# Kernel tuning notes

Measured on AMD Instinct MI355X. Metric: run time of the kernel, lower is better.

The kernel has to match this reference:

```python
import jax, jax.numpy as jnp
import numpy as np

EPS = 1e-8
INV_SQRT = 1.0 / np.sqrt(1.0 + EPS)  # 1/sqrt(|k|+eps), |k|=1 for both hyp and sph


def layernorm(x, w, b, eps=1e-5):
    m = jnp.mean(x, axis=-1, keepdims=True)
    v = jnp.mean((x - m) ** 2, axis=-1, keepdims=True)
    return (x - m) * jax.lax.rsqrt(v + eps) * w + b


def setup_inputs() -> dict:
    key = jax.random.key(0)
    B, S, D, H = 4, 1024, 512, 8
    d = D // H
    FF = 2048
    ks = jax.random.split(key, 12)
    s_attn = 1.0 / np.sqrt(d)
    s_d = 1.0 / np.sqrt(D)
    s_ff = 1.0 / np.sqrt(FF)
    return {
        "x": jax.random.normal(ks[0], (B, S, D), jnp.float32),
        "Wq": jax.random.normal(ks[1], (H, d, d), jnp.float32) * s_attn,
        "Wk": jax.random.normal(ks[2], (H, d, d), jnp.float32) * s_attn,
        "Wv": jax.random.normal(ks[3], (H, d, d), jnp.float32) * s_attn,
        "gw": jnp.ones((H, 3), jnp.float32) / 3.0,
        "temp": jnp.ones((H,), jnp.float32),
        "Wo": jax.random.normal(ks[4], (D, D), jnp.float32) * s_d,
        "bo": jnp.zeros((D,), jnp.float32),
        "ln1_w": jnp.ones((D,), jnp.float32),
        "ln1_b": jnp.zeros((D,), jnp.float32),
        "ln2_w": jnp.ones((D,), jnp.float32),
        "ln2_b": jnp.zeros((D,), jnp.float32),
        "W1": jax.random.normal(ks[5], (FF, D), jnp.float32) * s_d,
        "b1": jnp.zeros((FF,), jnp.float32),
        "W2": jax.random.normal(ks[6], (D, FF), jnp.float32) * s_ff,
        "b2": jnp.zeros((D,), jnp.float32),
    }


def reference(x, Wq, Wk, Wv, gw, temp, Wo, bo, ln1_w, ln1_b, ln2_w, ln2_b, W1, b1, W2, b2):
    B, S, D = x.shape
    H = Wq.shape[0]
    d = D // H

    h = layernorm(x, ln1_w, ln1_b)
    xh = h.reshape(B, S, H, d).transpose(0, 2, 1, 3)  # [B,H,S,d]
    # nn.Linear: y = x @ W^T
    q = jnp.einsum("bhsd,hed->bhse", xh, Wq)
    k = jnp.einsum("bhsd,hed->bhse", xh, Wk)
    v = jnp.einsum("bhsd,hed->bhse", xh, Wv)

    qsq = jnp.sum(q * q, axis=-1)  # [B,H,S] == ||q||^2
    ksq = jnp.sum(k * k, axis=-1)
    qk = jnp.einsum("bhsd,bhtd->bhst", q, k)
    # ||q-k||^2 via expansion (same math as sum(diff^2), avoids [B,H,S,S,d])
    dsq = jnp.maximum(qsq[..., :, None] + ksq[..., None, :] - 2.0 * qk, 0.0)
    euc = jnp.sqrt(dsq + EPS)

    denom = (1.0 - qsq)[..., :, None] * (1.0 - ksq)[..., None, :] + EPS
    cosh_arg = jnp.clip(1.0 + 2.0 * dsq / denom, 1.0, 1e6)
    hyp = jnp.arccosh(cosh_arg) * INV_SQRT

    qn = jnp.sqrt(qsq)
    kn = jnp.sqrt(ksq)
    cos_angle = qk / ((qn + EPS)[..., :, None] * (kn + EPS)[..., None, :])
    cos_angle = jnp.clip(cos_angle, -1.0 + EPS, 1.0 - EPS)
    sph = jnp.arccos(cos_angle) * INV_SQRT

    w = jax.nn.softmax(gw, axis=-1)  # [H,3] per-head geometry mixing
    comb = (
        w[:, 0, None, None] * hyp
        + w[:, 1, None, None] * euc
        + w[:, 2, None, None] * sph
    )
    sim = -comb * temp[None, :, None, None]
    attn = jax.nn.softmax(sim, axis=-1)
    out = jnp.einsum("bhst,bhtd->bhsd", attn, v)
    out = out.transpose(0, 2, 1, 3).reshape(B, S, D)
    attn_out = out @ Wo.T + bo

    x = x + attn_out  # dropout=0 (eval)
    h2 = layernorm(x, ln2_w, ln2_b)
    ff = jax.nn.gelu(h2 @ W1.T + b1, approximate=False) @ W2.T + b2
    return x + ff, w
```

## Files before the change

kernel.cpp:

```cpp
#include <hip/hip_runtime.h>
#include <hip/hip_bf16.h>
#include <math.h>

typedef __attribute__((ext_vector_type(4))) float f32x4;
typedef __attribute__((ext_vector_type(8))) short bf16x8;
typedef unsigned short u16;
typedef unsigned int u32;

typedef f32x4  __attribute__((may_alias)) f32x4a;
typedef bf16x8 __attribute__((may_alias)) bf16x8a;
typedef uint2  __attribute__((may_alias)) uint2a;

__device__ __forceinline__ u16 bfbits(float f) {
  union { __hip_bfloat16 h; u16 u; } cv;
  cv.h = __float2bfloat16(f);
  return cv.u;
}
__device__ __forceinline__ float rcp_r(float x)  { return __builtin_amdgcn_rcpf(x); }
__device__ __forceinline__ float sqrt_r(float x) { return __builtin_amdgcn_sqrtf(x); }
__device__ __forceinline__ float log2_r(float x) { return __builtin_amdgcn_logf(x); }
__device__ __forceinline__ float exp2_r(float x) { return __builtin_amdgcn_exp2f(x); }
__device__ __forceinline__ float rsq_r(float x)  { return __builtin_amdgcn_rsqf(x); }
__device__ __forceinline__ u32 cvt_pk_bf16(float lo, float hi) {
  u32 r;
  asm("v_cvt_pk_bf16_f32 %0, %1, %2" : "=v"(r) : "v"(lo), "v"(hi));
  return r;
}
typedef const __attribute__((address_space(1))) unsigned int* gas_t;
typedef __attribute__((address_space(3))) unsigned int* las_t;
__device__ __forceinline__ void gload_lds16(const u16* g, u16* l) {
  __builtin_amdgcn_global_load_lds((gas_t)g, (las_t)l, 16, 0, 0);
}

__global__ __launch_bounds__(256) void convert_weights(
    const float* __restrict__ wq, const float* __restrict__ wk, const float* __restrict__ wv,
    const float* __restrict__ wo, const float* __restrict__ w1, const float* __restrict__ w2,
    u16* __restrict__ owq, u16* __restrict__ owk, u16* __restrict__ owv,
    u16* __restrict__ owo, u16* __restrict__ ow1, u16* __restrict__ ow2) {
  int i = blockIdx.x * 256 + threadIdx.x;
  const float* src; u16* dst; int base;
  if (i < 8192)        { src = wq; dst = owq; base = 0; }
  else if (i < 16384)  { src = wk; dst = owk; base = 8192; }
  else if (i < 24576)  { src = wv; dst = owv; base = 16384; }
  else if (i < 90112)  { src = wo; dst = owo; base = 24576; }
  else if (i < 352256) { src = w1; dst = ow1; base = 90112; }
  else                 { src = w2; dst = ow2; base = 352256; }
  int li = i - base;
  float4 v = reinterpret_cast<const float4*>(src)[li];
  ushort4 o;
  o.x = bfbits(v.x); o.y = bfbits(v.y); o.z = bfbits(v.z); o.w = bfbits(v.w);
  reinterpret_cast<ushort4*>(dst)[li] = o;
}

__global__ __launch_bounds__(128) void ln_kernel(const float* __restrict__ x,
    const float* __restrict__ w, const float* __restrict__ b, u16* __restrict__ out) {
  int row = blockIdx.x, tid = threadIdx.x;
  float4 v = reinterpret_cast<const float4*>(x + row * 512)[tid];
  float s  = v.x + v.y + v.z + v.w;
  float s2 = v.x*v.x + v.y*v.y + v.z*v.z + v.w*v.w;
  #pragma unroll
  for (int o = 32; o > 0; o >>= 1) { s += __shfl_down(s, o); s2 += __shfl_down(s2, o); }
  __shared__ float sm[4];
  if ((tid & 63) == 0) { sm[(tid >> 6)*2] = s; sm[(tid >> 6)*2 + 1] = s2; }
  __syncthreads();
  float ts = sm[0] + sm[2], ts2 = sm[1] + sm[3];
  float mean = ts * (1.f/512.f);
  float var  = ts2 * (1.f/512.f) - mean*mean;
  float rstd = rsq_r(var + 1e-5f);
  float4 wv = reinterpret_cast<const float4*>(w)[tid];
  float4 bv = reinterpret_cast<const float4*>(b)[tid];
  ushort4 o;
  o.x = bfbits((v.x-mean)*rstd*wv.x + bv.x);
  o.y = bfbits((v.y-mean)*rstd*wv.y + bv.y);
  o.z = bfbits((v.z-mean)*rstd*wv.z + bv.z);
  o.w = bfbits((v.w-mean)*rstd*wv.w + bv.w);
  reinterpret_cast<ushort4*>(out + row * 512)[tid] = o;
}

__global__ __launch_bounds__(256) void qkv_kernel(const u16* __restrict__ h1,
    const u16* __restrict__ wqb, const u16* __restrict__ wkb, const u16* __restrict__ wvb,
    u16* __restrict__ q, u16* __restrict__ k, u16* __restrict__ vt,
    float* __restrict__ qsq, float* __restrict__ qom, float* __restrict__ qrs,
    float* __restrict__ ksq, float* __restrict__ kom, float* __restrict__ krs) {
  int mt = blockIdx.x, head = blockIdx.y;
  int wave = threadIdx.x >> 6, lane = threadIdx.x & 63;
  int lr = lane & 15, lg = lane >> 4;
  int m0 = mt * 64 + wave * 16;
  const u16* xr = h1 + (m0 + lr) * 512 + head * 64 + lg * 8;
  bf16x8 a0 = *reinterpret_cast<const bf16x8a*>(xr);
  bf16x8 a1 = *reinterpret_cast<const bf16x8a*>(xr + 32);
  int m_base = m0 + 4*lg;
  int bq = m_base >> 10;
  int s_base = m_base & 1023;
  int bh = (bq << 3) + head;
  #pragma unroll 1
  for (int mat = 0; mat < 3; ++mat) {
    const u16* W = (mat == 0 ? wqb : mat == 1 ? wkb : wvb) + head * 4096;
    f32x4 acc[4];
    #pragma unroll
    for (int c = 0; c < 4; c++)
      #pragma unroll
      for (int j = 0; j < 4; j++) acc[c][j] = 0.f;
    #pragma unroll
    for (int c = 0; c < 4; c++) {
      const u16* wr = W + (c*16 + lr) * 64 + lg * 8;
      bf16x8 b0 = *reinterpret_cast<const bf16x8a*>(wr);
      bf16x8 b1 = *reinterpret_cast<const bf16x8a*>(wr + 32);
      acc[c] = __builtin_amdgcn_mfma_f32_16x16x32_bf16(a0, b0, acc[c], 0, 0, 0);
      acc[c] = __builtin_amdgcn_mfma_f32_16x16x32_bf16(a1, b1, acc[c], 0, 0, 0);
    }
    if (mat == 2) {
      #pragma unroll
      for (int c = 0; c < 4; c++)
        #pragma unroll
        for (int j = 0; j < 4; j++)
          vt[(bh*64 + c*16 + lr) * 1024 + s_base + j] = bfbits(acc[c][j]);
    } else {
      u16* dst = (mat == 0 ? q : k);
      float* sq = (mat == 0 ? qsq : ksq);
      float* om = (mat == 0 ? qom : kom);
      float* rs = (mat == 0 ? qrs : krs);
      float ss[4] = {0.f, 0.f, 0.f, 0.f};
      #pragma unroll
      for (int c = 0; c < 4; c++)
        #pragma unroll
        for (int j = 0; j < 4; j++) {
          float vv = acc[c][j];
          dst[(bh*1024 + s_base + j) * 64 + c*16 + lr] = bfbits(vv);
          ss[j] += vv * vv;
        }
      #pragma unroll
      for (int j = 0; j < 4; j++) {
        #pragma unroll
        for (int o = 1; o < 16; o <<= 1) ss[j] += __shfl_xor(ss[j], o);
      }
      if (lr == 0) {
        #pragma unroll
        for (int j = 0; j < 4; j++) {
          float v = ss[j];
          int idx = bh*1024 + s_base + j;
          sq[idx] = v;
          om[idx] = rcp_r(1.f - v);
          rs[idx] = rsq_r(v);
        }
      }
    }
  }
}

__global__ __launch_bounds__(512, 4) void attn_kernel(
    const u16* __restrict__ q, const u16* __restrict__ k, const u16* __restrict__ vt,
    const float* __restrict__ qsqA, const float* __restrict__ qomA, const float* __restrict__ qrsA,
    const float* __restrict__ ksqA, const float* __restrict__ komA, const float* __restrict__ krsA,
    const float* __restrict__ gw, const float* __restrict__ temp,
    u16* __restrict__ attnb) {
  int bh = blockIdx.y;
  int b = bh >> 3, head = bh & 7;
  int tid = threadIdx.x;
  int wave = tid >> 6;
  int wq = wave & 1;
  int split = wave >> 1;
  int lane = tid & 63;
  int lr = lane & 15, lg = lane >> 4;
  int q0 = blockIdx.x * 32 + wq * 16;

  const u16* qp = q  + bh * 65536;
  const u16* kp = k  + bh * 65536;
  const u16* vp = vt + bh * 65536;

  __shared__ float ks_s[1024], kom_s[1024], rkn_s[1024];
  __shared__ __align__(16) u16 umem[5120];
  u16* pw = umem + wave * 640;

  for (int i = tid; i < 1024; i += 512) {
    ks_s[i]  = ksqA[(bh << 10) + i];
    kom_s[i] = komA[(bh << 10) + i];
    rkn_s[i] = krsA[(bh << 10) + i];
  }
  __syncthreads();

  float g0 = gw[head*3], g1 = gw[head*3+1], g2 = gw[head*3+2];
  float gm = fmaxf(g0, fmaxf(g1, g2));
  float e0 = __expf(g0-gm), e1 = __expf(g1-gm), e2 = __expf(g2-gm);
  float gi = rcp_r(e0 + e1 + e2);
  float tp = temp[head];
  const float LOG2E = 1.4426950408889634f;
  float chn = -e0*gi*tp;
  float cen = -e1*gi*tp*LOG2E;
  float csn = -e2*gi*tp*LOG2E;

  const u16* qr = qp + (q0 + lr) * 64 + lg * 8;
  bf16x8 aq0 = *reinterpret_cast<const bf16x8a*>(qr);
  bf16x8 aq1 = *reinterpret_cast<const bf16x8a*>(qr + 32);
  float qs   = qsqA[(bh << 10) + q0 + lr];
  float qom2 = 2.f * qomA[(bh << 10) + q0 + lr];
  float rqn  = qrsA[(bh << 10) + q0 + lr];

  f32x4 acc[4];
  #pragma unroll
  for (int c = 0; c < 4; c++)
    #pragma unroll
    for (int j = 0; j < 4; j++) acc[c][j] = 0.f;
  float psum0 = 0.f, psum1 = 0.f;

  for (int it = 0; it < 8; ++it) {
    int t0 = split * 256 + it * 32;
    const u16* kr = kp + (t0 + lr) * 64 + lg * 8;
    bf16x8 k00 = *reinterpret_cast<const bf16x8a*>(kr);
    bf16x8 k01 = *reinterpret_cast<const bf16x8a*>(kr + 32);
    bf16x8 k10 = *reinterpret_cast<const bf16x8a*>(kr + 1024);
    bf16x8 k11 = *reinterpret_cast<const bf16x8a*>(kr + 1024 + 32);
    f32x4 s0, s1;
    #pragma unroll
    for (int j = 0; j < 4; j++) { s0[j] = 0.f; s1[j] = 0.f; }
    s0 = __builtin_amdgcn_mfma_f32_16x16x32_bf16(k00, aq0, s0, 0, 0, 0);
    s0 = __builtin_amdgcn_mfma_f32_16x16x32_bf16(k01, aq1, s0, 0, 0, 0);
    s1 = __builtin_amdgcn_mfma_f32_16x16x32_bf16(k10, aq0, s1, 0, 0, 0);
    s1 = __builtin_amdgcn_mfma_f32_16x16x32_bf16(k11, aq1, s1, 0, 0, 0);

    f32x4 kq0 = *reinterpret_cast<const f32x4a*>(&ks_s[t0 + 4*lg]);
    f32x4 kq1 = *reinterpret_cast<const f32x4a*>(&ks_s[t0 + 16 + 4*lg]);
    f32x4 ko0 = *reinterpret_cast<const f32x4a*>(&kom_s[t0 + 4*lg]);
    f32x4 ko1 = *reinterpret_cast<const f32x4a*>(&kom_s[t0 + 16 + 4*lg]);
    f32x4 rk0 = *reinterpret_cast<const f32x4a*>(&rkn_s[t0 + 4*lg]);
    f32x4 rk1 = *reinterpret_cast<const f32x4a*>(&rkn_s[t0 + 16 + 4*lg]);

    float pv0[4], pv1[4];
    #pragma unroll
    for (int tc = 0; tc < 2; tc++) {
      f32x4 sv = tc ? s1 : s0;
      f32x4 kq = tc ? kq1 : kq0;
      f32x4 ko = tc ? ko1 : ko0;
      f32x4 rk = tc ? rk1 : rk0;
      float* pv = tc ? pv1 : pv0;
      #pragma unroll
      for (int j = 0; j < 4; j++) {
        float qk  = sv[j];
        float dsq = fmaxf(fmaf(qk, -2.f, qs + kq[j]), 0.f);
        float euc = sqrt_r(dsq);
        float u   = dsq * qom2 * ko[j];
        u = fminf(fmaxf(u, 0.f), 999999.f);
        float u2 = u + u;
        float sr = sqrt_r(fmaf(u, u, u2));
        float hyp2 = log2_r((u + 1.f) + sr);
        float ca = qk * rqn * rk[j];
        ca = fminf(fmaxf(ca, -1.f), 1.f);
        float aa = fabsf(ca);
        float pp = fmaf(aa, -0.0187293f, 0.0742610f);
        pp = fmaf(aa, pp, -0.2121144f);
        pp = fmaf(aa, pp, 1.5707288f);
        float rr = sqrt_r(1.f - aa) * pp;
        float sph = ca < 0.f ? 3.14159265358979f - rr : rr;
        float sim2 = fmaf(chn, hyp2, fmaf(cen, euc, csn * sph));
        float p = exp2_r(sim2);
        if (tc) psum1 += p; else psum0 += p;
        pv[j] = p;
      }
    }
    u32 w0 = cvt_pk_bf16(pv0[0], pv0[1]);
    u32 w1 = cvt_pk_bf16(pv0[2], pv0[3]);
    u32 w2 = cvt_pk_bf16(pv1[0], pv1[1]);
    u32 w3 = cvt_pk_bf16(pv1[2], pv1[3]);
    *reinterpret_cast<uint2a*>(pw + lr*40 + 4*lg)      = make_uint2(w0, w1);
    *reinterpret_cast<uint2a*>(pw + lr*40 + 16 + 4*lg) = make_uint2(w2, w3);
    bf16x8 pa = *reinterpret_cast<const bf16x8a*>(pw + lr*40 + lg*8);
    #pragma unroll
    for (int c = 0; c < 4; c++) {
      bf16x8 av = *reinterpret_cast<const bf16x8a*>(vp + (c*16 + lr)*1024 + t0 + lg*8);
      acc[c] = __builtin_amdgcn_mfma_f32_16x16x32_bf16(av, pa, acc[c], 0, 0, 0);
    }
  }

  float lt = psum0 + psum1;
  lt += __shfl_xor(lt, 16);
  lt += __shfl_xor(lt, 32);

  float* fa = (float*)umem;
  __syncthreads();
  #pragma unroll 1
  for (int s = 1; s <= 3; ++s) {
    int base = (wq*64 + lane)*20;
    if (split == s) {
      #pragma unroll
      for (int c = 0; c < 4; c++)
        *reinterpret_cast<f32x4a*>(fa + base + c*4) = acc[c];
      fa[base + 16] = lt;
    }
    __syncthreads();
    if (split == 0) {
      #pragma unroll
      for (int c = 0; c < 4; c++)
        acc[c] += *reinterpret_cast<const f32x4a*>(fa + base + c*4);
      lt += fa[base + 16];
    }
    __syncthreads();
  }
  if (split == 0) {
    float rl = rcp_r(lt);
    #pragma unroll
    for (int c = 0; c < 4; c++) {
      ushort4 st;
      st.x = bfbits(acc[c][0]*rl); st.y = bfbits(acc[c][1]*rl);
      st.z = bfbits(acc[c][2]*rl); st.w = bfbits(acc[c][3]*rl);
      *reinterpret_cast<ushort4*>(
          &attnb[(size_t)((b << 10) + q0 + lr) * 512 + head*64 + c*16 + 4*lg]) = st;
    }
  }
}

template<int K, int KS, int BM, int BN, int MODE>
__global__ __launch_bounds__(256, 2) void gemm_kernel(
    const u16* __restrict__ X, const u16* __restrict__ W,
    const float* __restrict__ bias, const float* __restrict__ res,
    float* __restrict__ outf, float* __restrict__ outf2, u16* __restrict__ outb) {
  constexpr int NS  = (MODE == 1) ? 2048 : 512;
  constexpr int WM  = (BM == 128 && BN == 128) ? 64 : 32;
  constexpr int WN  = (BN == 128 || BM == 128) ? 64 : 32;
  constexpr int NFR = WM / 16;
  constexpr int NFC = WN / 16;
  constexpr int NWC = BN / WN;
  constexpr int ACH = (BM * 4) / 256;
  constexpr int BCH = (BN * 4) / 256;
  __shared__ u16 As[BM * 32];
  __shared__ u16 Bs[BN * 32];
  int tid = threadIdx.x;
  int wave = tid >> 6, lane = tid & 63;
  int lr = lane & 15, lg = lane >> 4;
  int wr = (NWC == 2) ? (wave >> 1) : wave;
  int wc = (NWC == 2) ? (wave & 1) : 0;
  int m0 = blockIdx.x * BM, n0 = blockIdx.y * BN;
  const u16* Xp = X;
  const u16* Wp = W;
  if constexpr (MODE == 3) { Xp += blockIdx.z * K; Wp += blockIdx.z * K; }
  f32x4 acc[NFR][NFC];
  #pragma unroll
  for (int fr = 0; fr < NFR; fr++)
    #pragma unroll
    for (int fc = 0; fc < NFC; fc++)
      #pragma unroll
      for (int j = 0; j < 4; j++) acc[fr][fc][j] = 0.f;
  const u16* Ag[ACH]; u16* Al[ACH];
  const u16* Bg[BCH]; u16* Bl[BCH];
  #pragma unroll
  for (int i = 0; i < ACH; i++) {
    int cb = i * 256 + wave * 64;
    int c  = cb + lane;
    int row = c >> 2;
    int col = ((c & 3) ^ (row & 3)) << 3;
    Ag[i] = Xp + (size_t)(m0 + row) * KS + col;
    Al[i] = As + cb * 8;
  }
  #pragma unroll
  for (int i = 0; i < BCH; i++) {
    int cb = i * 256 + wave * 64;
    int c  = cb + lane;
    int row = c >> 2;
    int col = ((c & 3) ^ (row & 3)) << 3;
    Bg[i] = Wp + (size_t)(n0 + row) * KS + col;
    Bl[i] = Bs + cb * 8;
  }
  int rdcol = ((lg ^ (lr & 3)) << 3);
  for (int k0 = 0; k0 < K; k0 += 32) {
    __syncthreads();
    #pragma unroll
    for (int i = 0; i < ACH; i++) gload_lds16(Ag[i] + k0, Al[i]);
    #pragma unroll
    for (int i = 0; i < BCH; i++) gload_lds16(Bg[i] + k0, Bl[i]);
    __syncthreads();
    bf16x8 af[NFR], bf_[NFC];
    #pragma unroll
    for (int fr = 0; fr < NFR; fr++)
      af[fr] = *reinterpret_cast<const bf16x8a*>(As + (wr*WM + fr*16 + lr)*32 + rdcol);
    #pragma unroll
    for (int fc = 0; fc < NFC; fc++)
      bf_[fc] = *reinterpret_cast<const bf16x8a*>(Bs + (wc*WN + fc*16 + lr)*32 + rdcol);
    #pragma unroll
    for (int fr = 0; fr < NFR; fr++)
      #pragma unroll
      for (int fc = 0; fc < NFC; fc++)
        acc[fr][fc] = __builtin_amdgcn_mfma_f32_16x16x32_bf16(af[fr], bf_[fc], acc[fr][fc], 0, 0, 0);
  }
  float* po = nullptr;
  if constexpr (MODE == 3) po = blockIdx.z ? outf2 : outf;
  #pragma unroll
  for (int fr = 0; fr < NFR; fr++)
    #pragma unroll
    for (int fc = 0; fc < NFC; fc++) {
      int col = n0 + wc*WN + fc*16 + lr;
      float bb = (MODE == 3) ? 0.f : bias[col];
      #pragma unroll
      for (int j = 0; j < 4; j++) {
        int row = m0 + wr*WM + fr*16 + 4*lg + j;
        float v = acc[fr][fc][j] + bb;
        if constexpr (MODE == 0) {
          outf[(size_t)row*NS + col] = v + res[(size_t)row*NS + col];
        } else if constexpr (MODE == 1) {
          float t = v * fmaf(v*v, 0.035677408137f, 0.7978845608f);
          float g = v * rcp_r(1.f + exp2_r(-2.8853900817779268f * t));
          outb[(size_t)row*NS + col] = bfbits(g);
        } else {
          po[(size_t)row*512 + col] = v;
        }
      }
    }
}

__global__ __launch_bounds__(256) void ff2_combine(
    const float* __restrict__ p0, const float* __restrict__ p1,
    const float* __restrict__ bias, const float* __restrict__ res,
    float* __restrict__ out, const float* __restrict__ gw, float* __restrict__ wout) {
  int i = blockIdx.x * 256 + threadIdx.x;
  float4 a = reinterpret_cast<const float4*>(p0)[i];
  float4 b = reinterpret_cast<const float4*>(p1)[i];
  float4 r = reinterpret_cast<const float4*>(res)[i];
  int col4 = (i & 127) << 2;
  float4 bb = *reinterpret_cast<const float4*>(bias + col4);
  float4 o;
  o.x = a.x + b.x + r.x + bb.x;
  o.y = a.y + b.y + r.y + bb.y;
  o.z = a.z + b.z + r.z + bb.z;
  o.w = a.w + b.w + r.w + bb.w;
  reinterpret_cast<float4*>(out)[i] = o;
  if (blockIdx.x == 0 && threadIdx.x < 8) {
    int h = threadIdx.x;
    float a0 = gw[h*3], a1 = gw[h*3+1], a2 = gw[h*3+2];
    float m = fmaxf(a0, fmaxf(a1, a2));
    float x0 = __expf(a0-m), x1 = __expf(a1-m), x2 = __expf(a2-m);
    float inv = rcp_r(x0 + x1 + x2);
    wout[h*3+0] = x0*inv; wout[h*3+1] = x1*inv; wout[h*3+2] = x2*inv;
  }
}

extern "C" void kernel_launch(void* const* d_in, const int* in_sizes, int n_in,
                              void* d_out, int out_size, void* d_ws, size_t ws_size,
                              hipStream_t stream) {
  const float* x    = (const float*)d_in[0];
  const float* Wq   = (const float*)d_in[1];
  const float* Wk   = (const float*)d_in[2];
  const float* Wv   = (const float*)d_in[3];
  const float* gw   = (const float*)d_in[4];
  const float* temp = (const float*)d_in[5];
  const float* Wo   = (const float*)d_in[6];
  const float* bo   = (const float*)d_in[7];
  const float* ln1w = (const float*)d_in[8];
  const float* ln1b = (const float*)d_in[9];
  const float* ln2w = (const float*)d_in[10];
  const float* ln2b = (const float*)d_in[11];
  const float* W1   = (const float*)d_in[12];
  const float* b1   = (const float*)d_in[13];
  const float* W2   = (const float*)d_in[14];
  const float* b2   = (const float*)d_in[15];

  char* ws = (char*)d_ws;
  u16*  wqb  = (u16*)(ws + 0);
  u16*  wkb  = (u16*)(ws + 65536);
  u16*  wvb  = (u16*)(ws + 131072);
  u16*  wob  = (u16*)(ws + 196608);
  u16*  w1b  = (u16*)(ws + 720896);
  u16*  w2b  = (u16*)(ws + 2818048);
  u16*  h1b  = (u16*)(ws + 4915200);
  u16*  qb   = (u16*)(ws + 9109504);
  u16*  kb   = (u16*)(ws + 13303808);
  u16*  vtb  = (u16*)(ws + 17498112);
  float* qsq = (float*)(ws + 21692416);
  float* ksq = (float*)(ws + 21823488);
  float* qom = (float*)(ws + 21954560);
  float* qrs = (float*)(ws + 22085632);
  float* kom = (float*)(ws + 22216704);
  float* krs = (float*)(ws + 22347776);
  u16*  attnb= (u16*)(ws + 22478848);
  float* x1  = (float*)(ws + 26673152);
  u16*  h2b  = (u16*)(ws + 35061760);
  float* p1f = (float*)(ws + 35061760);
  u16*  gb   = (u16*)(ws + 4915200);

  float* outf = (float*)d_out;
  float* wout = outf + 4096*512;

  convert_weights<<<2400, 256, 0, stream>>>(Wq, Wk, Wv, Wo, W1, W2,
                                            wqb, wkb, wvb, wob, w1b, w2b);
  ln_kernel<<<4096, 128, 0, stream>>>(x, ln1w, ln1b, h1b);
  qkv_kernel<<<dim3(64, 8), 256, 0, stream>>>(h1b, wqb, wkb, wvb, qb, kb, vtb,
                                              qsq, qom, qrs, ksq, kom, krs);
  attn_kernel<<<dim3(32, 32), 512, 0, stream>>>(qb, kb, vtb, qsq, qom, qrs,
                                                ksq, kom, krs, gw, temp, attnb);
  gemm_kernel<512, 512, 64, 64, 0><<<dim3(64, 8), 256, 0, stream>>>(
      attnb, wob, bo, x, x1, nullptr, nullptr);
  ln_kernel<<<4096, 128, 0, stream>>>(x1, ln2w, ln2b, h2b);
  gemm_kernel<512, 512, 128, 128, 1><<<dim3(32, 16), 256, 0, stream>>>(
      h2b, w1b, b1, nullptr, nullptr, nullptr, gb);
  gemm_kernel<1024, 2048, 128, 64, 3><<<dim3(32, 8, 2), 256, 0, stream>>>(
      gb, w2b, nullptr, nullptr, outf, p1f, nullptr);
  ff2_combine<<<2048, 256, 0, stream>>>(outf, p1f, b2, x1, outf, gw, wout);
}
```

Baseline: 224.5 us.

## Prefetch K/V fragments in attention, vectorize V stores, fold bias+residual into FF2

In the attention loop, the next K tile is loaded one iteration early and the V fragments are loaded before the softmax math, so global-load latency overlaps with the exp/arccos/arccosh arithmetic. The QKV kernel writes transposed V with one 4-wide store per fragment instead of scalar stores. The FF2 split-K GEMM now adds the bias and residual in its z=0 partial, so the combine kernel reads only two arrays instead of four. These changes add register pressure in the attention kernel and may lower occupancy.

```diff
diff --git a/kernel.cpp b/kernel.cpp
--- a/kernel.cpp
+++ b/kernel.cpp
@@ -111,10 +111,12 @@
     }
     if (mat == 2) {
       #pragma unroll
-      for (int c = 0; c < 4; c++)
-        #pragma unroll
-        for (int j = 0; j < 4; j++)
-          vt[(bh*64 + c*16 + lr) * 1024 + s_base + j] = bfbits(acc[c][j]);
+      for (int c = 0; c < 4; c++) {
+        ushort4 st;
+        st.x = bfbits(acc[c][0]); st.y = bfbits(acc[c][1]);
+        st.z = bfbits(acc[c][2]); st.w = bfbits(acc[c][3]);
+        *reinterpret_cast<ushort4*>(&vt[(bh*64 + c*16 + lr) * 1024 + s_base]) = st;
+      }
     } else {
       u16* dst = (mat == 0 ? q : k);
       float* sq = (mat == 0 ? qsq : ksq);
@@ -203,20 +205,33 @@
     for (int j = 0; j < 4; j++) acc[c][j] = 0.f;
   float psum0 = 0.f, psum1 = 0.f;
 
+  const u16* kr0 = kp + (split * 256 + lr) * 64 + lg * 8;
+  bf16x8 kc0 = *reinterpret_cast<const bf16x8a*>(kr0);
+  bf16x8 kc1 = *reinterpret_cast<const bf16x8a*>(kr0 + 32);
+  bf16x8 kc2 = *reinterpret_cast<const bf16x8a*>(kr0 + 1024);
+  bf16x8 kc3 = *reinterpret_cast<const bf16x8a*>(kr0 + 1024 + 32);
+
   for (int it = 0; it < 8; ++it) {
     int t0 = split * 256 + it * 32;
-    const u16* kr = kp + (t0 + lr) * 64 + lg * 8;
-    bf16x8 k00 = *reinterpret_cast<const bf16x8a*>(kr);
-    bf16x8 k01 = *reinterpret_cast<const bf16x8a*>(kr + 32);
-    bf16x8 k10 = *reinterpret_cast<const bf16x8a*>(kr + 1024);
-    bf16x8 k11 = *reinterpret_cast<const bf16x8a*>(kr + 1024 + 32);
     f32x4 s0, s1;
     #pragma unroll
     for (int j = 0; j < 4; j++) { s0[j] = 0.f; s1[j] = 0.f; }
-    s0 = __builtin_amdgcn_mfma_f32_16x16x32_bf16(k00, aq0, s0, 0, 0, 0);
-    s0 = __builtin_amdgcn_mfma_f32_16x16x32_bf16(k01, aq1, s0, 0, 0, 0);
-    s1 = __builtin_amdgcn_mfma_f32_16x16x32_bf16(k10, aq0, s1, 0, 0, 0);
-    s1 = __builtin_amdgcn_mfma_f32_16x16x32_bf16(k11, aq1, s1, 0, 0, 0);
+    s0 = __builtin_amdgcn_mfma_f32_16x16x32_bf16(kc0, aq0, s0, 0, 0, 0);
+    s0 = __builtin_amdgcn_mfma_f32_16x16x32_bf16(kc1, aq1, s0, 0, 0, 0);
+    s1 = __builtin_amdgcn_mfma_f32_16x16x32_bf16(kc2, aq0, s1, 0, 0, 0);
+    s1 = __builtin_amdgcn_mfma_f32_16x16x32_bf16(kc3, aq1, s1, 0, 0, 0);
+
+    if (it < 7) {
+      const u16* krn = kp + (t0 + 32 + lr) * 64 + lg * 8;
+      kc0 = *reinterpret_cast<const bf16x8a*>(krn);
+      kc1 = *reinterpret_cast<const bf16x8a*>(krn + 32);
+      kc2 = *reinterpret_cast<const bf16x8a*>(krn + 1024);
+      kc3 = *reinterpret_cast<const bf16x8a*>(krn + 1024 + 32);
+    }
+    bf16x8 av[4];
+    #pragma unroll
+    for (int c = 0; c < 4; c++)
+      av[c] = *reinterpret_cast<const bf16x8a*>(vp + (c*16 + lr)*1024 + t0 + lg*8);
 
     f32x4 kq0 = *reinterpret_cast<const f32x4a*>(&ks_s[t0 + 4*lg]);
     f32x4 kq1 = *reinterpret_cast<const f32x4a*>(&ks_s[t0 + 16 + 4*lg]);
@@ -265,10 +280,8 @@
     *reinterpret_cast<uint2a*>(pw + lr*40 + 16 + 4*lg) = make_uint2(w2, w3);
     bf16x8 pa = *reinterpret_cast<const bf16x8a*>(pw + lr*40 + lg*8);
     #pragma unroll
-    for (int c = 0; c < 4; c++) {
-      bf16x8 av = *reinterpret_cast<const bf16x8a*>(vp + (c*16 + lr)*1024 + t0 + lg*8);
-      acc[c] = __builtin_amdgcn_mfma_f32_16x16x32_bf16(av, pa, acc[c], 0, 0, 0);
-    }
+    for (int c = 0; c < 4; c++)
+      acc[c] = __builtin_amdgcn_mfma_f32_16x16x32_bf16(av[c], pa, acc[c], 0, 0, 0);
   }
 
   float lt = psum0 + psum1;
@@ -381,7 +394,8 @@
         acc[fr][fc] = __builtin_amdgcn_mfma_f32_16x16x32_bf16(af[fr], bf_[fc], acc[fr][fc], 0, 0, 0);
   }
   float* po = nullptr;
-  if constexpr (MODE == 3) po = blockIdx.z ? outf2 : outf;
+  bool z0 = true;
+  if constexpr (MODE == 3) { z0 = (blockIdx.z == 0); po = z0 ? outf : outf2; }
   #pragma unroll
   for (int fr = 0; fr < NFR; fr++)
     #pragma unroll
@@ -399,6 +413,7 @@
           float g = v * rcp_r(1.f + exp2_r(-2.8853900817779268f * t));
           outb[(size_t)row*NS + col] = bfbits(g);
         } else {
+          if (z0) v += bias[col] + res[(size_t)row*512 + col];
           po[(size_t)row*512 + col] = v;
         }
       }
@@ -407,19 +422,15 @@
 
 __global__ __launch_bounds__(256) void ff2_combine(
     const float* __restrict__ p0, const float* __restrict__ p1,
-    const float* __restrict__ bias, const float* __restrict__ res,
     float* __restrict__ out, const float* __restrict__ gw, float* __restrict__ wout) {
   int i = blockIdx.x * 256 + threadIdx.x;
   float4 a = reinterpret_cast<const float4*>(p0)[i];
   float4 b = reinterpret_cast<const float4*>(p1)[i];
-  float4 r = reinterpret_cast<const float4*>(res)[i];
-  int col4 = (i & 127) << 2;
-  float4 bb = *reinterpret_cast<const float4*>(bias + col4);
   float4 o;
-  o.x = a.x + b.x + r.x + bb.x;
-  o.y = a.y + b.y + r.y + bb.y;
-  o.z = a.z + b.z + r.z + bb.z;
-  o.w = a.w + b.w + r.w + bb.w;
+  o.x = a.x + b.x;
+  o.y = a.y + b.y;
+  o.z = a.z + b.z;
+  o.w = a.w + b.w;
   reinterpret_cast<float4*>(out)[i] = o;
   if (blockIdx.x == 0 && threadIdx.x < 8) {
     int h = threadIdx.x;
@@ -490,6 +501,6 @@
   gemm_kernel<512, 512, 128, 128, 1><<<dim3(32, 16), 256, 0, stream>>>(
       h2b, w1b, b1, nullptr, nullptr, nullptr, gb);
   gemm_kernel<1024, 2048, 128, 64, 3><<<dim3(32, 8, 2), 256, 0, stream>>>(
-      gb, w2b, nullptr, nullptr, outf, p1f, nullptr);
-  ff2_combine<<<2048, 256, 0, stream>>>(outf, p1f, b2, x1, outf, gw, wout);
-}
+      gb, w2b, b2, x1, outf, p1f, nullptr);
+  ff2_combine<<<2048, 256, 0, stream>>>(outf, p1f, outf, gw, wout);
+}
```

Result: no change. 228.0 us (+1.6%).
